# Kernel optimization log

Hardware: AMD Instinct MI355X
Metric: run time of the kernel (lower is better)

Reference implementation:

```python
import jax, jax.numpy as jnp
import numpy as np

B, S, D = 2, 2048, 2048
G, HPG = 4, 4            # n_groups, heads_per_group (n_heads=16)
DH = D // (G * HPG)      # head dim d_q = d_k = d_v = 128


def setup_inputs() -> dict:
    key = jax.random.key(0)
    ks = jax.random.split(key, 14)
    s = 1.0 / np.sqrt(D)
    inp = {
        "query": jax.random.normal(ks[0], (B, S, D), jnp.float32),
        "key":   jax.random.normal(ks[1], (B, S, D), jnp.float32),
        "value": jax.random.normal(ks[2], (B, S, D), jnp.float32),
        # per-group, per-head Q projections; per-group shared K, V
        "WQ": jax.random.normal(ks[3], (G, HPG, DH, D), jnp.float32) * s,
        "bQ": jax.random.normal(ks[4], (G, HPG, DH), jnp.float32) * 0.01,
        "WK": jax.random.normal(ks[5], (G, DH, D), jnp.float32) * s,
        "bK": jax.random.normal(ks[6], (G, DH), jnp.float32) * 0.01,
        "WV": jax.random.normal(ks[7], (G, DH, D), jnp.float32) * s,
        "bV": jax.random.normal(ks[8], (G, DH), jnp.float32) * 0.01,
        "WO": jax.random.normal(ks[9], (D, G * HPG * DH), jnp.float32) * s,
        "bO": jax.random.normal(ks[10], (D,), jnp.float32) * 0.01,
    }
    return inp


def reference(query, key, value, WQ, bQ, WK, bK, WV, bV, WO, bO):
    # q: [B, G, HPG, S, DH] — all per-head Q projections as one batched GEMM
    q = jnp.einsum('bsd,ghqd->bghsq', query, WQ) + bQ[None, :, :, None, :]
    # k, v: [B, G, S, DH] — one K/V per group (shared across heads in group)
    k = jnp.einsum('bsd,gkd->bgsk', key, WK) + bK[None, :, None, :]
    v = jnp.einsum('bsd,gvd->bgsv', value, WV) + bV[None, :, None, :]
    scale = 1.0 / jnp.sqrt(jnp.asarray(DH, q.dtype))
    # scores: [B, G, HPG, S_q, S_k]
    scores = jnp.einsum('bghsq,bgtq->bghst', q, k) * scale
    attn = jax.nn.softmax(scores, axis=-1)
    out = jnp.einsum('bghst,bgtv->bghsv', attn, v)   # [B, G, HPG, S, DH]
    # concat heads group-major, then transpose(1,2) + flatten like the torch code
    out = out.reshape(B, G * HPG, S, DH).transpose(0, 2, 1, 3).reshape(B, S, G * HPG * DH)
    return out @ WO.T + bO
```

## Files before the change

kernel.cpp:

```cpp
#include <hip/hip_runtime.h>
#include <cstdint>
#include <cstddef>


typedef __attribute__((ext_vector_type(8)))  __bf16 bf16x8;
typedef __attribute__((ext_vector_type(4)))  __bf16 bf16x4;
typedef __attribute__((ext_vector_type(4)))  float  f32x4;
typedef __attribute__((ext_vector_type(16))) float  f32x16;
typedef __attribute__((ext_vector_type(4)))  unsigned int u32x4;

#define GLD16(gp, lp) __builtin_amdgcn_global_load_lds(                         \
    (__attribute__((address_space(1))) void*)(size_t)(gp),                     \
    (__attribute__((address_space(3))) void*)(lp), 16, 0, 0)

#define PLSWAP(a, b) asm volatile("v_permlane32_swap_b32 %0, %1" : "+v"(a), "+v"(b))
#define EXP2F(x) __builtin_amdgcn_exp2f(x)

static __device__ __forceinline__ unsigned pack2bf(float a, float b) {
    unsigned short ua = __builtin_bit_cast(unsigned short, (__bf16)a);
    unsigned short ub = __builtin_bit_cast(unsigned short, (__bf16)b);
    return (unsigned)ua | ((unsigned)ub << 16);
}

struct F2BArgs {
    const float* src[7];
    __bf16* dst[7];
    long beg[8];
};
__global__ void f2b_multi(F2BArgs a) {
    const long total = a.beg[7];
    const long stride = (long)gridDim.x * blockDim.x;
    for (long i = (long)blockIdx.x * blockDim.x + threadIdx.x; i < total; i += stride) {
        int s = 0;
#pragma unroll
        for (int j = 1; j < 7; ++j) s += (i >= a.beg[j]);
        long off = i - a.beg[s];
        const float4* p = (const float4*)(a.src[s] + off * 8);
        float4 x = p[0], y = p[1];
        bf16x8 r;
        r[0] = (__bf16)x.x; r[1] = (__bf16)x.y; r[2] = (__bf16)x.z; r[3] = (__bf16)x.w;
        r[4] = (__bf16)y.x; r[5] = (__bf16)y.y; r[6] = (__bf16)y.z; r[7] = (__bf16)y.w;
        *(bf16x8*)(a.dst[s] + off * 8) = r;
    }
}

template <int OUTF32>
__global__ __launch_bounds__(512)
void gemm256(const __bf16* __restrict__ A, const __bf16* __restrict__ Bm,
             const float* __restrict__ bias, float* __restrict__ Cf,
             __bf16* __restrict__ Cb, int M, int N, int K, int nbx) {
    __shared__ __bf16 As[3][256 * 64];
    __shared__ __bf16 Bs[3][128 * 64];
    const int tid = threadIdx.x, lane = tid & 63, wid = tid >> 6;
    const int g = lane >> 4, c = lane & 15;
    const int wr = wid >> 1, wc = wid & 1;
    const int cpx = gridDim.x >> 3;
    const int swz = ((int)blockIdx.x & 7) * cpx + ((int)blockIdx.x >> 3);
    const int bx = swz % nbx, by = swz / nbx;
    const int m0 = by * 256, n0 = bx * 128;
    const int nkt = K >> 6;

    const f32x4 z = {0.f, 0.f, 0.f, 0.f};
    f32x4 acc[4][4];
#pragma unroll
    for (int i = 0; i < 4; ++i)
#pragma unroll
        for (int j = 0; j < 4; ++j) acc[i][j] = z;

    auto stageA = [&](int b, int kt, int h) {
        if (kt >= nkt) return;
        const __bf16* src = A + (size_t)m0 * K + (size_t)kt * 64;
#pragma unroll
        for (int i = 0; i < 2; ++i) {
            int ci = h * 1024 + i * 512 + tid;
            int row = ci >> 3, chg = (ci & 7) ^ (row & 7);
            GLD16(src + (size_t)row * K + chg * 8, &As[b][ci * 8]);
        }
    };
    auto stageB = [&](int b, int kt) {
        if (kt >= nkt) return;
        const __bf16* src = Bm + (size_t)n0 * K + (size_t)kt * 64;
#pragma unroll
        for (int i = 0; i < 2; ++i) {
            int ci = i * 512 + tid;
            int row = ci >> 3, chg = (ci & 7) ^ (row & 7);
            GLD16(src + (size_t)row * K + chg * 8, &Bs[b][ci * 8]);
        }
    };

    stageA(0, 0, 0); stageA(0, 0, 1); stageB(0, 0);
    stageA(1, 1, 0); stageA(1, 1, 1); stageB(1, 1);
    asm volatile("s_waitcnt vmcnt(6)" ::: "memory");
    __builtin_amdgcn_sched_barrier(0);
    __builtin_amdgcn_s_barrier();

    int bd = 0;
    for (int kt = 0; kt < nkt; ++kt) {
        const int bs = (bd >= 1) ? bd - 1 : 2;
        bf16x8 af[4], bfr[4];
#pragma unroll
        for (int ph = 0; ph < 2; ++ph) {
#pragma unroll
            for (int mi = 0; mi < 4; ++mi) {
                int row = wr * 64 + mi * 16 + c;
                int ch = (ph * 4 + g) ^ (c & 7);
                af[mi] = *(const bf16x8*)&As[bd][row * 64 + ch * 8];
            }
#pragma unroll
            for (int ni = 0; ni < 4; ++ni) {
                int row = wc * 64 + ni * 16 + c;
                int ch = (ph * 4 + g) ^ (c & 7);
                bfr[ni] = *(const bf16x8*)&Bs[bd][row * 64 + ch * 8];
            }
            if (ph == 0) {
                stageA(bs, kt + 2, 0);
            } else {
                stageA(bs, kt + 2, 1);
                stageB(bs, kt + 2);
            }
            __builtin_amdgcn_s_barrier();
            asm volatile("s_waitcnt lgkmcnt(0)" ::: "memory");
            __builtin_amdgcn_sched_barrier(0);
            __builtin_amdgcn_s_setprio(1);
#pragma unroll
            for (int mi = 0; mi < 4; ++mi)
#pragma unroll
                for (int ni = 0; ni < 4; ++ni)
                    acc[mi][ni] = __builtin_amdgcn_mfma_f32_16x16x32_bf16(
                        af[mi], bfr[ni], acc[mi][ni], 0, 0, 0);
            __builtin_amdgcn_s_setprio(0);
            if (ph == 1) {
                if (kt >= nkt - 2) asm volatile("s_waitcnt vmcnt(0)" ::: "memory");
                else               asm volatile("s_waitcnt vmcnt(6)" ::: "memory");
                __builtin_amdgcn_sched_barrier(0);
            }
            __builtin_amdgcn_s_barrier();
        }
        bd = (bd >= 2) ? 0 : bd + 1;
    }

#pragma unroll
    for (int mi = 0; mi < 4; ++mi) {
#pragma unroll
        for (int ni = 0; ni < 4; ++ni) {
            int col = n0 + wc * 64 + ni * 16 + c;
            float bvc = bias[col];
#pragma unroll
            for (int r = 0; r < 4; ++r) {
                int row = m0 + wr * 64 + mi * 16 + g * 4 + r;
                float v = acc[mi][ni][r] + bvc;
                if (OUTF32) Cf[(size_t)row * N + col] = v;
                else        Cb[(size_t)row * N + col] = (__bf16)v;
            }
        }
    }
}

static __device__ __forceinline__
void gemm_tile(const __bf16* __restrict__ A, const __bf16* __restrict__ Bm,
               const float* __restrict__ bias,
               __bf16* __restrict__ Cb, int N, int K, int m0, int n0, int biasrow,
               __bf16* As, __bf16* Bs) {
    const int tid = threadIdx.x;
    const int lane = tid & 63, wid = tid >> 6;
    const int g = lane >> 4, c = lane & 15;
    const int wr = wid >> 1, wc = wid & 1;

    const f32x4 z = {0.f, 0.f, 0.f, 0.f};
    f32x4 acc[4][4];
#pragma unroll
    for (int i = 0; i < 4; ++i)
#pragma unroll
        for (int j = 0; j < 4; ++j) acc[i][j] = z;

    const int nk = K >> 5;
#pragma unroll
    for (int i = 0; i < 2; ++i) {
        int ci = i * 256 + tid, row = ci >> 2, kc = (ci & 3) * 8;
        GLD16(A + (size_t)(m0 + row) * K + kc, As + ci * 8);
        GLD16(Bm + (size_t)(n0 + row) * K + kc, Bs + ci * 8);
    }
    __syncthreads();

    int cur = 0;
    for (int t = 0; t < nk; ++t) {
        if (t + 1 < nk) {
            int koff = (t + 1) * 32;
            int nb = (cur ^ 1) * 4096;
#pragma unroll
            for (int i = 0; i < 2; ++i) {
                int ci = i * 256 + tid, row = ci >> 2, kc = (ci & 3) * 8;
                GLD16(A + (size_t)(m0 + row) * K + koff + kc, As + nb + ci * 8);
                GLD16(Bm + (size_t)(n0 + row) * K + koff + kc, Bs + nb + ci * 8);
            }
        }
        int cb = cur * 4096;
        bf16x8 af[4], bfv[4];
#pragma unroll
        for (int im = 0; im < 4; ++im)
            af[im] = *(const bf16x8*)&As[cb + (wr * 64 + im * 16 + c) * 32 + g * 8];
#pragma unroll
        for (int in = 0; in < 4; ++in)
            bfv[in] = *(const bf16x8*)&Bs[cb + (wc * 64 + in * 16 + c) * 32 + g * 8];
        __builtin_amdgcn_s_setprio(1);
#pragma unroll
        for (int im = 0; im < 4; ++im)
#pragma unroll
            for (int in = 0; in < 4; ++in)
                acc[im][in] = __builtin_amdgcn_mfma_f32_16x16x32_bf16(
                    af[im], bfv[in], acc[im][in], 0, 0, 0);
        __builtin_amdgcn_s_setprio(0);
        __syncthreads();
        cur ^= 1;
    }

#pragma unroll
    for (int im = 0; im < 4; ++im) {
#pragma unroll
        for (int in = 0; in < 4; ++in) {
            int col = n0 + wc * 64 + in * 16 + c;
            float bvc = biasrow ? 0.f : bias[col];
#pragma unroll
            for (int r = 0; r < 4; ++r) {
                int row = m0 + wr * 64 + im * 16 + g * 4 + r;
                float v = acc[im][in][r] + (biasrow ? bias[row] : bvc);
                Cb[(size_t)row * N + col] = (__bf16)v;
            }
        }
    }
}

__global__ __launch_bounds__(256)
void gemm_kv(const __bf16* __restrict__ kb, const __bf16* __restrict__ wkb,
             const float* __restrict__ bK, __bf16* __restrict__ kp,
             const __bf16* __restrict__ wvb, const __bf16* __restrict__ vb,
             const float* __restrict__ bV, __bf16* __restrict__ vpT) {
    __shared__ __bf16 As[2 * 128 * 32];
    __shared__ __bf16 Bs[2 * 128 * 32];
    const int bid = blockIdx.x;
    const int swz = (bid & 7) * 32 + (bid >> 3);
    if (swz < 128) {
        int bx = swz & 31, by = swz >> 5;
        gemm_tile(kb, wkb, bK, kp, 512, 2048, bx * 128, by * 128, 0, As, Bs);
    } else {
        int s2 = swz - 128;
        int bx = s2 & 3, by = s2 >> 2;
        gemm_tile(wvb, vb, bV, vpT, 4096, 2048, bx * 128, by * 128, 1, As, Bs);
    }
}

__global__ __launch_bounds__(256)
void attn_kernel(const __bf16* __restrict__ Qw, const __bf16* __restrict__ Kw,
                 const __bf16* __restrict__ VTw, __bf16* __restrict__ Ow) {
    constexpr int S = 2048, DQ = 2048, DKV = 512, TOK = 4096;
    constexpr int nt = S / 32;
    const int bid = blockIdx.x;
    const int xcd = bid & 7, slot = bid >> 3;
    const int b = xcd >> 2, grp = xcd & 3;
    const int head = grp * 4 + (slot & 3);
    const int qblk = slot >> 2;
    const int t0 = slot & (nt - 1);
    const __bf16* Q   = Qw + (size_t)b * S * DQ + head * 128;
    const __bf16* Kp  = Kw + (size_t)b * S * DKV + grp * 128;
    const __bf16* VTp = VTw + (size_t)(grp * 128) * TOK + (size_t)b * S;
    __bf16* Op = Ow + (size_t)b * S * DQ + head * 128;

    __shared__ __bf16 Ks[3][32 * 128];
    __shared__ __bf16 Vs[3][128 * 32];

    const int tid = threadIdx.x, wid = tid >> 6, lane = tid & 63;
    const int ql = lane & 31, hi = lane >> 5;
    const int qrow = qblk * 128 + wid * 32 + ql;

    bf16x8 qf[8];
#pragma unroll
    for (int ks = 0; ks < 8; ++ks)
        qf[ks] = *(const bf16x8*)(Q + (size_t)qrow * DQ + ks * 16 + hi * 8);

    f32x16 o[4];
#pragma unroll
    for (int d = 0; d < 4; ++d)
#pragma unroll
        for (int r = 0; r < 16; ++r) o[d][r] = 0.f;
    float mprev = -1e30f, lsum = 0.f;
    constexpr float kexp = 0.08838834764831845f * 1.4426950408889634f;
    constexpr float THR = 8.0f / kexp;

    auto stage = [&](int buf, int t) {
#pragma unroll
        for (int i = 0; i < 2; ++i) {
            int ci = i * 256 + tid;
            int key = ci >> 4, ccl = ci & 15, ccg = ccl ^ (key & 15);
            GLD16(Kp + (size_t)(t * 32 + key) * DKV + ccg * 8, &Ks[buf][ci * 8]);
        }
#pragma unroll
        for (int i = 0; i < 2; ++i) {
            int ci = i * 256 + tid;
            int dh = ci >> 2, cl = ci & 3, cg = cl ^ ((dh >> 1) & 3);
            GLD16(VTp + (size_t)dh * TOK + t * 32 + cg * 8, &Vs[buf][ci * 8]);
        }
    };

    stage(0, t0);
    stage(1, (t0 + 1) & (nt - 1));
    asm volatile("s_waitcnt vmcnt(4)" ::: "memory");
    asm volatile("s_barrier" ::: "memory");

    int bc = 0;
    for (int i = 0; i < nt; ++i) {
        const int bs = (bc >= 1) ? bc - 1 : 2;
        if (i + 2 < nt) stage(bs, (t0 + i + 2) & (nt - 1));

        f32x16 sc;
#pragma unroll
        for (int r = 0; r < 16; ++r) sc[r] = 0.f;
        __builtin_amdgcn_s_setprio(1);
#pragma unroll
        for (int ks = 0; ks < 8; ++ks) {
            int chl = (ks * 2 + hi) ^ (ql & 15);
            bf16x8 kf = *(const bf16x8*)&Ks[bc][ql * 128 + chl * 8];
            sc = __builtin_amdgcn_mfma_f32_32x32x16_bf16(kf, qf[ks], sc, 0, 0, 0);
        }
        __builtin_amdgcn_s_setprio(0);

        float mo = sc[0];
#pragma unroll
        for (int r = 1; r < 16; ++r) mo = fmaxf(mo, sc[r]);
        mo = fmaxf(mo, __shfl_xor(mo, 32, 64));
        if (!__all(mo - mprev <= THR)) {
            float mn = fmaxf(mprev, mo);
            float ef = EXP2F((mprev - mn) * kexp);
            lsum *= ef;
#pragma unroll
            for (int d = 0; d < 4; ++d)
#pragma unroll
                for (int r = 0; r < 16; ++r) o[d][r] *= ef;
            mprev = mn;
        }
        float mnk = mprev * kexp;
        float rs = 0.f;
#pragma unroll
        for (int r = 0; r < 16; ++r) {
            float p = EXP2F(__builtin_fmaf(sc[r], kexp, -mnk));
            sc[r] = p;
            rs += p;
        }
        rs += __shfl_xor(rs, 32, 64);
        lsum += rs;

        unsigned pk[4][2];
#pragma unroll
        for (int rg = 0; rg < 4; ++rg) {
            pk[rg][0] = pack2bf(sc[rg * 4 + 0], sc[rg * 4 + 1]);
            pk[rg][1] = pack2bf(sc[rg * 4 + 2], sc[rg * 4 + 3]);
        }

        __builtin_amdgcn_s_setprio(1);
#pragma unroll
        for (int e = 0; e < 2; ++e) {
            unsigned a0 = pk[2 * e][0], b0 = pk[2 * e + 1][0];
            unsigned a1 = pk[2 * e][1], b1 = pk[2 * e + 1][1];
            PLSWAP(a0, b0);
            PLSWAP(a1, b1);
            u32x4 fw = {a0, a1, b0, b1};
            bf16x8 pf = __builtin_bit_cast(bf16x8, fw);
#pragma unroll
            for (int dht = 0; dht < 4; ++dht) {
                int dh = dht * 32 + ql;
                int chl = (e * 2 + hi) ^ ((dh >> 1) & 3);
                bf16x8 vf = *(const bf16x8*)&Vs[bc][dh * 32 + chl * 8];
                o[dht] = __builtin_amdgcn_mfma_f32_32x32x16_bf16(vf, pf, o[dht], 0, 0, 0);
            }
        }
        __builtin_amdgcn_s_setprio(0);

        if (i + 2 < nt) asm volatile("s_waitcnt vmcnt(4)" ::: "memory");
        else            asm volatile("s_waitcnt vmcnt(0)" ::: "memory");
        asm volatile("s_barrier" ::: "memory");
        bc = (bc >= 2) ? 0 : bc + 1;
    }

    float inv = 1.0f / lsum;
#pragma unroll
    for (int dht = 0; dht < 4; ++dht)
#pragma unroll
        for (int rg = 0; rg < 4; ++rg) {
            bf16x4 wv;
#pragma unroll
            for (int j = 0; j < 4; ++j) wv[j] = (__bf16)(o[dht][rg * 4 + j] * inv);
            int dh0 = dht * 32 + rg * 8 + hi * 4;
            *(bf16x4*)(Op + (size_t)qrow * DQ + dh0) = wv;
        }
}

extern "C" void kernel_launch(void* const* d_in, const int* in_sizes, int n_in,
                              void* d_out, int out_size, void* d_ws, size_t ws_size,
                              hipStream_t stream) {
    (void)in_sizes; (void)n_in; (void)out_size; (void)ws_size;
    const float* query = (const float*)d_in[0];
    const float* key   = (const float*)d_in[1];
    const float* value = (const float*)d_in[2];
    const float* WQ = (const float*)d_in[3];
    const float* bQ = (const float*)d_in[4];
    const float* WK = (const float*)d_in[5];
    const float* bK = (const float*)d_in[6];
    const float* WV = (const float*)d_in[7];
    const float* bV = (const float*)d_in[8];
    const float* WO = (const float*)d_in[9];
    const float* bO = (const float*)d_in[10];
    float* out = (float*)d_out;

    __bf16* w = (__bf16*)d_ws;
    __bf16* qb  = w; w += (size_t)4096 * 2048;
    __bf16* kb  = w; w += (size_t)4096 * 2048;
    __bf16* vb  = w; w += (size_t)4096 * 2048;
    __bf16* wqb = w; w += (size_t)2048 * 2048;
    __bf16* wkb = w; w += (size_t)512 * 2048;
    __bf16* wvb = w; w += (size_t)512 * 2048;
    __bf16* wob = w; w += (size_t)2048 * 2048;
    __bf16* qp  = w; w += (size_t)4096 * 2048;
    __bf16* kp  = w; w += (size_t)4096 * 512;
    __bf16* vpT = w; w += (size_t)512 * 4096;
    __bf16* ao  = w; w += (size_t)4096 * 2048;

    F2BArgs fa;
    fa.src[0] = query; fa.dst[0] = qb;
    fa.src[1] = key;   fa.dst[1] = kb;
    fa.src[2] = value; fa.dst[2] = vb;
    fa.src[3] = WQ;    fa.dst[3] = wqb;
    fa.src[4] = WK;    fa.dst[4] = wkb;
    fa.src[5] = WV;    fa.dst[5] = wvb;
    fa.src[6] = WO;    fa.dst[6] = wob;
    const long n8s[7] = {1048576, 1048576, 1048576, 524288, 131072, 131072, 524288};
    long acc = 0;
    for (int i = 0; i < 7; ++i) { fa.beg[i] = acc; acc += n8s[i]; }
    fa.beg[7] = acc;
    f2b_multi<<<2048, 256, 0, stream>>>(fa);

    gemm256<0><<<256, 512, 0, stream>>>(qb, wqb, bQ, nullptr, qp, 4096, 2048, 2048, 16);
    gemm_kv<<<256, 256, 0, stream>>>(kb, wkb, bK, kp, wvb, vb, bV, vpT);

    attn_kernel<<<512, 256, 0, stream>>>(qp, kp, vpT, ao);

    gemm256<1><<<256, 512, 0, stream>>>(ao, wob, bO, out, nullptr, 4096, 2048, 2048, 16);
}
```

Measured before the change: 262.1 us.

## Split attention key range across two wave groups per block and merge partial softmax

The attention kernel now launches 512 threads per block. Two groups of four waves each process half of the key sequence (split-K within the block) and merge their partial online-softmax states through shared memory at the end. Staging moves from triple to double buffering with a new LDS swizzle for the wider V tiles. The aim is more waves in flight per CU to hide latency, at the cost of a merge step, more LDS use, and a full vmcnt(0) wait every iteration.

```diff
diff --git a/kernel.cpp b/kernel.cpp
--- a/kernel.cpp
+++ b/kernel.cpp
@@ -249,11 +249,11 @@
     }
 }
 
-__global__ __launch_bounds__(256)
+__global__ __launch_bounds__(512, 4)
 void attn_kernel(const __bf16* __restrict__ Qw, const __bf16* __restrict__ Kw,
                  const __bf16* __restrict__ VTw, __bf16* __restrict__ Ow) {
     constexpr int S = 2048, DQ = 2048, DKV = 512, TOK = 4096;
-    constexpr int nt = S / 32;
+    constexpr int nt = 32;
     const int bid = blockIdx.x;
     const int xcd = bid & 7, slot = bid >> 3;
     const int b = xcd >> 2, grp = xcd & 3;
@@ -265,12 +265,16 @@
     const __bf16* VTp = VTw + (size_t)(grp * 128) * TOK + (size_t)b * S;
     __bf16* Op = Ow + (size_t)b * S * DQ + head * 128;
 
-    __shared__ __bf16 Ks[3][32 * 128];
-    __shared__ __bf16 Vs[3][128 * 32];
+    __shared__ __align__(16) char smem[65536];
+    __shared__ float mlx[4][64][2];
+    __bf16* Ks = (__bf16*)smem;
+    __bf16* Vs = (__bf16*)(smem + 32768);
 
     const int tid = threadIdx.x, wid = tid >> 6, lane = tid & 63;
     const int ql = lane & 31, hi = lane >> 5;
-    const int qrow = qblk * 128 + wid * 32 + ql;
+    const int g = wid >> 2;
+    const int qrow = qblk * 128 + (wid & 3) * 32 + ql;
+    const int kbase = g * 1024;
 
     bf16x8 qf[8];
 #pragma unroll
@@ -287,29 +291,31 @@
     constexpr float THR = 8.0f / kexp;
 
     auto stage = [&](int buf, int t) {
+        int ta = (t0 + t) & (nt - 1);
 #pragma unroll
         for (int i = 0; i < 2; ++i) {
-            int ci = i * 256 + tid;
+            int ci = i * 512 + tid;
             int key = ci >> 4, ccl = ci & 15, ccg = ccl ^ (key & 15);
-            GLD16(Kp + (size_t)(t * 32 + key) * DKV + ccg * 8, &Ks[buf][ci * 8]);
+            int gk = (key & 31) + ta * 32 + ((key >> 5) << 10);
+            GLD16(Kp + (size_t)gk * DKV + ccg * 8, &Ks[buf * 8192 + ci * 8]);
         }
 #pragma unroll
         for (int i = 0; i < 2; ++i) {
-            int ci = i * 256 + tid;
-            int dh = ci >> 2, cl = ci & 3, cg = cl ^ ((dh >> 1) & 3);
-            GLD16(VTp + (size_t)dh * TOK + t * 32 + cg * 8, &Vs[buf][ci * 8]);
+            int ci = i * 512 + tid;
+            int dh = ci >> 3, cl = ci & 7;
+            int cg = cl ^ ((dh ^ (dh >> 3)) & 7);
+            int gko = ((cg >> 2) << 10) + ta * 32 + (cg & 3) * 8;
+            GLD16(VTp + (size_t)dh * TOK + gko, &Vs[buf * 8192 + ci * 8]);
         }
     };
 
-    stage(0, t0);
-    stage(1, (t0 + 1) & (nt - 1));
-    asm volatile("s_waitcnt vmcnt(4)" ::: "memory");
+    stage(0, 0);
+    asm volatile("s_waitcnt vmcnt(0)" ::: "memory");
     asm volatile("s_barrier" ::: "memory");
 
-    int bc = 0;
+    int cur = 0;
     for (int i = 0; i < nt; ++i) {
-        const int bs = (bc >= 1) ? bc - 1 : 2;
-        if (i + 2 < nt) stage(bs, (t0 + i + 2) & (nt - 1));
+        if (i + 1 < nt) stage(cur ^ 1, i + 1);
 
         f32x16 sc;
 #pragma unroll
@@ -317,8 +323,9 @@
         __builtin_amdgcn_s_setprio(1);
 #pragma unroll
         for (int ks = 0; ks < 8; ++ks) {
+            int key_l = g * 32 + ql;
             int chl = (ks * 2 + hi) ^ (ql & 15);
-            bf16x8 kf = *(const bf16x8*)&Ks[bc][ql * 128 + chl * 8];
+            bf16x8 kf = *(const bf16x8*)&Ks[cur * 8192 + key_l * 128 + chl * 8];
             sc = __builtin_amdgcn_mfma_f32_32x32x16_bf16(kf, qf[ks], sc, 0, 0, 0);
         }
         __builtin_amdgcn_s_setprio(0);
@@ -367,30 +374,53 @@
 #pragma unroll
             for (int dht = 0; dht < 4; ++dht) {
                 int dh = dht * 32 + ql;
-                int chl = (e * 2 + hi) ^ ((dh >> 1) & 3);
-                bf16x8 vf = *(const bf16x8*)&Vs[bc][dh * 32 + chl * 8];
+                int chl = (g * 4 + e * 2 + hi) ^ ((dh ^ (dh >> 3)) & 7);
+                bf16x8 vf = *(const bf16x8*)&Vs[cur * 8192 + dh * 64 + chl * 8];
                 o[dht] = __builtin_amdgcn_mfma_f32_32x32x16_bf16(vf, pf, o[dht], 0, 0, 0);
             }
         }
         __builtin_amdgcn_s_setprio(0);
 
-        if (i + 2 < nt) asm volatile("s_waitcnt vmcnt(4)" ::: "memory");
-        else            asm volatile("s_waitcnt vmcnt(0)" ::: "memory");
+        asm volatile("s_waitcnt vmcnt(0)" ::: "memory");
         asm volatile("s_barrier" ::: "memory");
-        bc = (bc >= 2) ? 0 : bc + 1;
-    }
-
-    float inv = 1.0f / lsum;
-#pragma unroll
-    for (int dht = 0; dht < 4; ++dht)
-#pragma unroll
-        for (int rg = 0; rg < 4; ++rg) {
-            bf16x4 wv;
-#pragma unroll
-            for (int j = 0; j < 4; ++j) wv[j] = (__bf16)(o[dht][rg * 4 + j] * inv);
-            int dh0 = dht * 32 + rg * 8 + hi * 4;
-            *(bf16x4*)(Op + (size_t)qrow * DQ + dh0) = wv;
-        }
+        cur ^= 1;
+    }
+
+    float4* ox = (float4*)smem;
+    if (g == 1) {
+        int w4 = wid & 3;
+#pragma unroll
+        for (int dht = 0; dht < 4; ++dht)
+#pragma unroll
+            for (int rg = 0; rg < 4; ++rg) {
+                float4 v = {o[dht][rg * 4 + 0], o[dht][rg * 4 + 1],
+                            o[dht][rg * 4 + 2], o[dht][rg * 4 + 3]};
+                ox[((w4 * 16 + dht * 4 + rg) << 6) + lane] = v;
+            }
+        mlx[w4][lane][0] = mprev;
+        mlx[w4][lane][1] = lsum;
+    }
+    __syncthreads();
+    if (g == 0) {
+        float m2 = mlx[wid][lane][0], l2 = mlx[wid][lane][1];
+        float mF = fmaxf(mprev, m2);
+        float e1 = EXP2F((mprev - mF) * kexp);
+        float e2 = EXP2F((m2 - mF) * kexp);
+        float linv = 1.0f / (lsum * e1 + l2 * e2);
+#pragma unroll
+        for (int dht = 0; dht < 4; ++dht)
+#pragma unroll
+            for (int rg = 0; rg < 4; ++rg) {
+                float4 p = ox[((wid * 16 + dht * 4 + rg) << 6) + lane];
+                bf16x4 wv;
+                wv[0] = (__bf16)((o[dht][rg * 4 + 0] * e1 + p.x * e2) * linv);
+                wv[1] = (__bf16)((o[dht][rg * 4 + 1] * e1 + p.y * e2) * linv);
+                wv[2] = (__bf16)((o[dht][rg * 4 + 2] * e1 + p.z * e2) * linv);
+                wv[3] = (__bf16)((o[dht][rg * 4 + 3] * e1 + p.w * e2) * linv);
+                int dh0 = dht * 32 + rg * 8 + hi * 4;
+                *(bf16x4*)(Op + (size_t)qrow * DQ + dh0) = wv;
+            }
+    }
 }
 
 extern "C" void kernel_launch(void* const* d_in, const int* in_sizes, int n_in,
@@ -440,7 +470,7 @@
     gemm256<0><<<256, 512, 0, stream>>>(qb, wqb, bQ, nullptr, qp, 4096, 2048, 2048, 16);
     gemm_kv<<<256, 256, 0, stream>>>(kb, wkb, bK, kp, wvb, vb, bV, vpT);
 
-    attn_kernel<<<512, 256, 0, stream>>>(qp, kp, vpT, ao);
+    attn_kernel<<<512, 512, 0, stream>>>(qp, kp, vpT, ao);
 
     gemm256<1><<<256, 512, 0, stream>>>(ao, wob, bO, out, nullptr, 4096, 2048, 2048, 16);
 }
```

After: 344.7 us. 1.32x slower.

## Merge Q, K, V projection GEMMs into one launch using 256x128 pipelined tiles

Applied to the files above, without the earlier changes.

Turns the triple-buffered 256x128 GEMM into a device body and launches Q, K and V^T projections together as one 384-block kernel. The K/V projections previously used a smaller double-buffered 128x128 kernel and now use the larger tile body. This removes one launch and lets the smaller K/V work fill the tail of the Q GEMM wave. The cost is a heterogeneous grid with uneven work per XCD, and large LDS use per block.

```diff
diff --git a/kernel.cpp b/kernel.cpp
--- a/kernel.cpp
+++ b/kernel.cpp
@@ -45,19 +45,14 @@
 }
 
 template <int OUTF32>
-__global__ __launch_bounds__(512)
-void gemm256(const __bf16* __restrict__ A, const __bf16* __restrict__ Bm,
-             const float* __restrict__ bias, float* __restrict__ Cf,
-             __bf16* __restrict__ Cb, int M, int N, int K, int nbx) {
-    __shared__ __bf16 As[3][256 * 64];
-    __shared__ __bf16 Bs[3][128 * 64];
+static __device__ __forceinline__
+void gemm256_body(const __bf16* __restrict__ A, const __bf16* __restrict__ Bm,
+                  const float* __restrict__ bias, float* __restrict__ Cf,
+                  __bf16* __restrict__ Cb, int N, int K, int m0, int n0,
+                  int biasrow, __bf16* As, __bf16* Bs) {
     const int tid = threadIdx.x, lane = tid & 63, wid = tid >> 6;
     const int g = lane >> 4, c = lane & 15;
     const int wr = wid >> 1, wc = wid & 1;
-    const int cpx = gridDim.x >> 3;
-    const int swz = ((int)blockIdx.x & 7) * cpx + ((int)blockIdx.x >> 3);
-    const int bx = swz % nbx, by = swz / nbx;
-    const int m0 = by * 256, n0 = bx * 128;
     const int nkt = K >> 6;
 
     const f32x4 z = {0.f, 0.f, 0.f, 0.f};
@@ -74,7 +69,7 @@
         for (int i = 0; i < 2; ++i) {
             int ci = h * 1024 + i * 512 + tid;
             int row = ci >> 3, chg = (ci & 7) ^ (row & 7);
-            GLD16(src + (size_t)row * K + chg * 8, &As[b][ci * 8]);
+            GLD16(src + (size_t)row * K + chg * 8, &As[b * 16384 + ci * 8]);
         }
     };
     auto stageB = [&](int b, int kt) {
@@ -84,7 +79,7 @@
         for (int i = 0; i < 2; ++i) {
             int ci = i * 512 + tid;
             int row = ci >> 3, chg = (ci & 7) ^ (row & 7);
-            GLD16(src + (size_t)row * K + chg * 8, &Bs[b][ci * 8]);
+            GLD16(src + (size_t)row * K + chg * 8, &Bs[b * 8192 + ci * 8]);
         }
     };
 
@@ -104,13 +99,13 @@
             for (int mi = 0; mi < 4; ++mi) {
                 int row = wr * 64 + mi * 16 + c;
                 int ch = (ph * 4 + g) ^ (c & 7);
-                af[mi] = *(const bf16x8*)&As[bd][row * 64 + ch * 8];
+                af[mi] = *(const bf16x8*)&As[bd * 16384 + row * 64 + ch * 8];
             }
 #pragma unroll
             for (int ni = 0; ni < 4; ++ni) {
                 int row = wc * 64 + ni * 16 + c;
                 int ch = (ph * 4 + g) ^ (c & 7);
-                bfr[ni] = *(const bf16x8*)&Bs[bd][row * 64 + ch * 8];
+                bfr[ni] = *(const bf16x8*)&Bs[bd * 8192 + row * 64 + ch * 8];
             }
             if (ph == 0) {
                 stageA(bs, kt + 2, 0);
@@ -144,11 +139,11 @@
 #pragma unroll
         for (int ni = 0; ni < 4; ++ni) {
             int col = n0 + wc * 64 + ni * 16 + c;
-            float bvc = bias[col];
+            float bvc = biasrow ? 0.f : bias[col];
 #pragma unroll
             for (int r = 0; r < 4; ++r) {
                 int row = m0 + wr * 64 + mi * 16 + g * 4 + r;
-                float v = acc[mi][ni][r] + bvc;
+                float v = acc[mi][ni][r] + (biasrow ? bias[row] : bvc);
                 if (OUTF32) Cf[(size_t)row * N + col] = v;
                 else        Cb[(size_t)row * N + col] = (__bf16)v;
             }
@@ -156,97 +151,44 @@
     }
 }
 
-static __device__ __forceinline__
-void gemm_tile(const __bf16* __restrict__ A, const __bf16* __restrict__ Bm,
-               const float* __restrict__ bias,
-               __bf16* __restrict__ Cb, int N, int K, int m0, int n0, int biasrow,
-               __bf16* As, __bf16* Bs) {
-    const int tid = threadIdx.x;
-    const int lane = tid & 63, wid = tid >> 6;
-    const int g = lane >> 4, c = lane & 15;
-    const int wr = wid >> 1, wc = wid & 1;
-
-    const f32x4 z = {0.f, 0.f, 0.f, 0.f};
-    f32x4 acc[4][4];
-#pragma unroll
-    for (int i = 0; i < 4; ++i)
-#pragma unroll
-        for (int j = 0; j < 4; ++j) acc[i][j] = z;
-
-    const int nk = K >> 5;
-#pragma unroll
-    for (int i = 0; i < 2; ++i) {
-        int ci = i * 256 + tid, row = ci >> 2, kc = (ci & 3) * 8;
-        GLD16(A + (size_t)(m0 + row) * K + kc, As + ci * 8);
-        GLD16(Bm + (size_t)(n0 + row) * K + kc, Bs + ci * 8);
-    }
-    __syncthreads();
-
-    int cur = 0;
-    for (int t = 0; t < nk; ++t) {
-        if (t + 1 < nk) {
-            int koff = (t + 1) * 32;
-            int nb = (cur ^ 1) * 4096;
-#pragma unroll
-            for (int i = 0; i < 2; ++i) {
-                int ci = i * 256 + tid, row = ci >> 2, kc = (ci & 3) * 8;
-                GLD16(A + (size_t)(m0 + row) * K + koff + kc, As + nb + ci * 8);
-                GLD16(Bm + (size_t)(n0 + row) * K + koff + kc, Bs + nb + ci * 8);
-            }
-        }
-        int cb = cur * 4096;
-        bf16x8 af[4], bfv[4];
-#pragma unroll
-        for (int im = 0; im < 4; ++im)
-            af[im] = *(const bf16x8*)&As[cb + (wr * 64 + im * 16 + c) * 32 + g * 8];
-#pragma unroll
-        for (int in = 0; in < 4; ++in)
-            bfv[in] = *(const bf16x8*)&Bs[cb + (wc * 64 + in * 16 + c) * 32 + g * 8];
-        __builtin_amdgcn_s_setprio(1);
-#pragma unroll
-        for (int im = 0; im < 4; ++im)
-#pragma unroll
-            for (int in = 0; in < 4; ++in)
-                acc[im][in] = __builtin_amdgcn_mfma_f32_16x16x32_bf16(
-                    af[im], bfv[in], acc[im][in], 0, 0, 0);
-        __builtin_amdgcn_s_setprio(0);
-        __syncthreads();
-        cur ^= 1;
-    }
-
-#pragma unroll
-    for (int im = 0; im < 4; ++im) {
-#pragma unroll
-        for (int in = 0; in < 4; ++in) {
-            int col = n0 + wc * 64 + in * 16 + c;
-            float bvc = biasrow ? 0.f : bias[col];
-#pragma unroll
-            for (int r = 0; r < 4; ++r) {
-                int row = m0 + wr * 64 + im * 16 + g * 4 + r;
-                float v = acc[im][in][r] + (biasrow ? bias[row] : bvc);
-                Cb[(size_t)row * N + col] = (__bf16)v;
-            }
-        }
-    }
-}
-
-__global__ __launch_bounds__(256)
-void gemm_kv(const __bf16* __restrict__ kb, const __bf16* __restrict__ wkb,
-             const float* __restrict__ bK, __bf16* __restrict__ kp,
-             const __bf16* __restrict__ wvb, const __bf16* __restrict__ vb,
-             const float* __restrict__ bV, __bf16* __restrict__ vpT) {
-    __shared__ __bf16 As[2 * 128 * 32];
-    __shared__ __bf16 Bs[2 * 128 * 32];
+__global__ __launch_bounds__(512)
+void gemm_proj(const __bf16* __restrict__ qb, const __bf16* __restrict__ wqb,
+               const float* __restrict__ bQ, __bf16* __restrict__ qp,
+               const __bf16* __restrict__ kb, const __bf16* __restrict__ wkb,
+               const float* __restrict__ bK, __bf16* __restrict__ kp,
+               const __bf16* __restrict__ wvb, const __bf16* __restrict__ vb,
+               const float* __restrict__ bV, __bf16* __restrict__ vpT) {
+    __shared__ __bf16 As[3 * 256 * 64];
+    __shared__ __bf16 Bs[3 * 128 * 64];
+    const int bid = blockIdx.x;
+    const int swz = (bid & 7) * 48 + (bid >> 3);
+    if (swz < 256) {
+        int bx = swz & 15, by = swz >> 4;
+        gemm256_body<0>(qb, wqb, bQ, nullptr, qp, 2048, 2048,
+                        by * 256, bx * 128, 0, As, Bs);
+    } else if (swz < 320) {
+        int s = swz - 256;
+        int bx = s & 3, by = s >> 2;
+        gemm256_body<0>(kb, wkb, bK, nullptr, kp, 512, 2048,
+                        by * 256, bx * 128, 0, As, Bs);
+    } else {
+        int s = swz - 320;
+        int bx = s & 31, by = s >> 5;
+        gemm256_body<0>(wvb, vb, bV, nullptr, vpT, 4096, 2048,
+                        by * 256, bx * 128, 1, As, Bs);
+    }
+}
+
+__global__ __launch_bounds__(512)
+void gemm_out(const __bf16* __restrict__ A, const __bf16* __restrict__ Bm,
+              const float* __restrict__ bias, float* __restrict__ Cf) {
+    __shared__ __bf16 As[3 * 256 * 64];
+    __shared__ __bf16 Bs[3 * 128 * 64];
     const int bid = blockIdx.x;
     const int swz = (bid & 7) * 32 + (bid >> 3);
-    if (swz < 128) {
-        int bx = swz & 31, by = swz >> 5;
-        gemm_tile(kb, wkb, bK, kp, 512, 2048, bx * 128, by * 128, 0, As, Bs);
-    } else {
-        int s2 = swz - 128;
-        int bx = s2 & 3, by = s2 >> 2;
-        gemm_tile(wvb, vb, bV, vpT, 4096, 2048, bx * 128, by * 128, 1, As, Bs);
-    }
+    int bx = swz & 15, by = swz >> 4;
+    gemm256_body<1>(A, Bm, bias, Cf, nullptr, 2048, 2048,
+                    by * 256, bx * 128, 0, As, Bs);
 }
 
 __global__ __launch_bounds__(256)
@@ -437,10 +379,11 @@
     fa.beg[7] = acc;
     f2b_multi<<<2048, 256, 0, stream>>>(fa);
 
-    gemm256<0><<<256, 512, 0, stream>>>(qb, wqb, bQ, nullptr, qp, 4096, 2048, 2048, 16);
-    gemm_kv<<<256, 256, 0, stream>>>(kb, wkb, bK, kp, wvb, vb, bV, vpT);
+    gemm_proj<<<384, 512, 0, stream>>>(qb, wqb, bQ, qp,
+                                       kb, wkb, bK, kp,
+                                       wvb, vb, bV, vpT);
 
     attn_kernel<<<512, 256, 0, stream>>>(qp, kp, vpT, ao);
 
-    gemm256<1><<<256, 512, 0, stream>>>(ao, wob, bO, out, nullptr, 4096, 2048, 2048, 16);
-}
+    gemm_out<<<256, 512, 0, stream>>>(ao, wob, bO, out);
+}
```

After: 252.4 us. 3.7% less time.
